# Performance work log

Hardware: AMD Instinct MI355X
Metric: run time of the kernel (lower is better)

The kernel has to match this reference:

```python
import jax, jax.numpy as jnp
import numpy as np

B, S, H = 2, 2048, 2048
NH, NKV, HD = 16, 4, 128
THETA = 10000.0


def _rope_cos_sin(seq_len, head_dim, theta, dtype):
    inv_freq = 1.0 / (theta ** (jnp.arange(0, head_dim, 2, dtype=jnp.float32) / head_dim))
    t = jnp.arange(seq_len, dtype=jnp.float32)
    freqs = t[:, None] * inv_freq[None, :]          # [S, HD/2]
    emb = jnp.concatenate([freqs, freqs], axis=-1)  # [S, HD]
    return jnp.cos(emb).astype(dtype), jnp.sin(emb).astype(dtype)


def _rotate_half(x):
    d = x.shape[-1] // 2
    return jnp.concatenate([-x[..., d:], x[..., :d]], axis=-1)


def setup_inputs() -> dict:
    key = jax.random.key(0)
    ks = jax.random.split(key, 5)
    x = jax.random.normal(ks[0], (B, S, H), dtype=jnp.float32)
    Wq = jax.random.normal(ks[1], (NH * HD, H), dtype=jnp.float32) * 0.02
    Wk = jax.random.normal(ks[2], (NKV * HD, H), dtype=jnp.float32) * 0.02
    Wv = jax.random.normal(ks[3], (NKV * HD, H), dtype=jnp.float32) * 0.02
    Wo = jax.random.normal(ks[4], (H, H), dtype=jnp.float32) * 0.02
    causal = jnp.tril(jnp.ones((S, S), dtype=bool))
    attention_mask = jnp.where(causal, 0.0, -1e9).astype(jnp.float32)[None, None]  # [1,1,S,S]
    return {"x": x, "attention_mask": attention_mask, "Wq": Wq, "Wk": Wk, "Wv": Wv, "Wo": Wo}


def reference(x, attention_mask, Wq, Wk, Wv, Wo):
    b, s, _ = x.shape
    q = (x @ Wq.T).reshape(b, s, NH, HD).transpose(0, 2, 1, 3)    # [b,nh,s,hd]
    k = (x @ Wk.T).reshape(b, s, NKV, HD).transpose(0, 2, 1, 3)   # [b,nkv,s,hd]
    v = (x @ Wv.T).reshape(b, s, NKV, HD).transpose(0, 2, 1, 3)
    cos, sin = _rope_cos_sin(s, HD, THETA, x.dtype)               # [s,hd] each
    cos = cos[None, None]; sin = sin[None, None]
    q = q * cos + _rotate_half(q) * sin
    k = k * cos + _rotate_half(k) * sin
    rep = NH // NKV
    k = jnp.repeat(k, rep, axis=1)                                 # [b,nh,s,hd]
    v = jnp.repeat(v, rep, axis=1)
    scores = jnp.einsum('bhqd,bhkd->bhqk', q, k) / jnp.sqrt(jnp.asarray(HD, x.dtype))
    scores = scores + attention_mask
    attn = jax.nn.softmax(scores, axis=-1)
    out = jnp.einsum('bhqk,bhkd->bhqd', attn, v)                   # [b,nh,s,hd]
    out = out.transpose(0, 2, 1, 3).reshape(b, s, NH * HD)
    return out @ Wo.T
```

## Files before the change

kernel.cpp:

```cpp
#include <hip/hip_runtime.h>

typedef unsigned short u16;
typedef __bf16 bf16x8 __attribute__((ext_vector_type(8)));
typedef float f32x4 __attribute__((ext_vector_type(4)));
typedef short s16x4 __attribute__((ext_vector_type(4)));

#define S_LEN  2048
#define NHEADS 16
#define NKVH   4
#define HDIM   128
#define BB     2
#define MROWS  4096
#define QKV_N  3072
#define HID    2048

__device__ __forceinline__ u16 f2b(float f) {
  union { float f; unsigned u; } x; x.f = f;
  unsigned r = x.u + 0x7fffu + ((x.u >> 16) & 1u);
  return (u16)(r >> 16);
}
__device__ __forceinline__ float b2f(u16 v) {
  union { unsigned u; float f; } x; x.u = ((unsigned)v) << 16;
  return x.f;
}
__device__ __forceinline__ void gload_lds16(const u16* g, u16* l) {
  __builtin_amdgcn_global_load_lds((__attribute__((address_space(1))) void*)g,
                                   (__attribute__((address_space(3))) void*)l,
                                   16, 0, 0);
}
__device__ __forceinline__ unsigned cvtpk(float lo, float hi) {
  unsigned r;
  asm("v_cvt_pk_bf16_f32 %0, %1, %2" : "=v"(r) : "v"(lo), "v"(hi));
  return r;
}
#if __has_builtin(__builtin_amdgcn_mfma_f32_16x16x16bf16_1k)
__device__ __forceinline__ f32x4 mfma16(s16x4 a, s16x4 b, f32x4 c) {
  return __builtin_amdgcn_mfma_f32_16x16x16bf16_1k(a, b, c, 0, 0, 0);
}
#else
__device__ __forceinline__ f32x4 mfma16(s16x4 a, s16x4 b, f32x4 c) {
  f32x4 d;
  asm volatile("v_mfma_f32_16x16x16_bf16 %0, %1, %2, %3"
               : "=v"(d) : "v"(a), "v"(b), "v"(c));
  return d;
}
#endif

#define SBAR() do { __builtin_amdgcn_sched_barrier(0); \
                    __builtin_amdgcn_s_barrier();      \
                    __builtin_amdgcn_sched_barrier(0); } while (0)

#define PB_X   8192
#define PB_WQ  (PB_X + 4096)
#define PB_WK  (PB_WQ + 1024)
#define PB_WV  (PB_WK + 1024)
#define PB_WO  (PB_WV + 4096)
#define PB_CS  (PB_WO + 512)
__global__ void k_prep(const float* __restrict__ x,
                       const float* __restrict__ Wq, const float* __restrict__ Wk,
                       const float* __restrict__ Wv, const float* __restrict__ Wo,
                       u16* __restrict__ xb, u16* __restrict__ Wqkvb,
                       u16* __restrict__ Wob, float* __restrict__ cs)
{
  const int bid = blockIdx.x, tid = threadIdx.x;
  const float* src; u16* dst; int i;
  if (bid < PB_X)       { i = bid * 256 + tid;            src = x;  dst = xb; }
  else if (bid < PB_WQ) { i = (bid - PB_X) * 256 + tid;   src = Wq; dst = Wqkvb; }
  else if (bid < PB_WK) { i = (bid - PB_WQ) * 256 + tid;  src = Wk; dst = Wqkvb + (size_t)2048 * HID; }
  else if (bid < PB_WV) { i = (bid - PB_WK) * 256 + tid;  src = Wv; dst = Wqkvb + (size_t)2560 * HID; }
  else if (bid < PB_WO) { i = (bid - PB_WV) * 256 + tid;  src = Wo; dst = Wob; }
  else {
    const int p = (bid - PB_WO) * 256 + tid;
    const int s = p >> 6, j = p & 63;
    float inv = expf(-(float)j * 0.14391156831212787f);
    float ang = (float)s * inv;
    float c, sn; sincosf(ang, &sn, &c);
    cs[p * 2 + 0] = c; cs[p * 2 + 1] = sn;
    return;
  }
  float4 v = ((const float4*)src)[i];
  ushort4 o;
  o.x = f2b(v.x); o.y = f2b(v.y); o.z = f2b(v.z); o.w = f2b(v.w);
  ((ushort4*)dst)[i] = o;
}

#define MFMA_GRP(AV, BV, MO, NO)                                              \
  __builtin_amdgcn_s_setprio(1);                                              \
  _Pragma("unroll") for (int kk = 0; kk < 2; ++kk)                            \
  _Pragma("unroll") for (int mm = 0; mm < 4; ++mm)                            \
  _Pragma("unroll") for (int nn = 0; nn < 2; ++nn)                            \
    acc[(MO) + mm][(NO) + nn] = __builtin_amdgcn_mfma_f32_16x16x32_bf16(      \
        AV[kk][mm], BV[kk][nn], acc[(MO) + mm][(NO) + nn], 0, 0, 0);          \
  __builtin_amdgcn_s_setprio(0);

template <int OUT_BF16>
__global__ __launch_bounds__(512, 2) void k_gemm256(
    const u16* __restrict__ A, const u16* __restrict__ Bm, void* __restrict__ Cv,
    int M, int N, int K)
{
  __shared__ u16 AL[2][2][8192];
  __shared__ u16 BL[2][2][8192];
  const int tid = threadIdx.x;
  const int wave = tid >> 6, lane = tid & 63;
  const int l15 = lane & 15, l4 = lane >> 4;
  const int wr = wave >> 2, wc = wave & 3;
  const int gx = gridDim.x;
  const int nwg = gx * gridDim.y;
  int bid = blockIdx.y * gx + blockIdx.x;
  bid = (bid & 7) * (nwg >> 3) + (bid >> 3);
  const int col0 = (bid % gx) * 256, row0 = (bid / gx) * 256;

  int srcOff[2], dstD[2];
#pragma unroll
  for (int li = 0; li < 2; ++li) {
    const int D = (li * 512 + tid) * 16;
    const int off_p = D & 1023, si = D >> 10;
    const int off_l = off_p ^ (((off_p >> 9) & 1) << 5);
    const int R = si >> 1, C = si & 1;
    const int row = R * 16 + (off_l >> 6);
    const int colb = C * 64 + (off_l & 63);
    srcOff[li] = row * K + (colb >> 1);
    dstD[li] = D;
  }
  const int laneoff = (l15 * 64 + l4 * 16) ^ ((l15 >> 3) << 5);

  auto stage = [&](const u16* __restrict__ G, int grow0, int kb, u16* lds) {
#pragma unroll
    for (int li = 0; li < 2; ++li)
      gload_lds16(G + (size_t)grow0 * K + kb + srcOff[li],
                  (u16*)((char*)lds + dstD[li]));
  };

  f32x4 acc[8][4];
#pragma unroll
  for (int m = 0; m < 8; ++m)
#pragma unroll
    for (int n = 0; n < 4; ++n) acc[m][n] = f32x4{0.f, 0.f, 0.f, 0.f};

  const int nk = K >> 6;
  stage(A,  row0,       0,  &AL[0][0][0]);
  stage(A,  row0 + 128, 0,  &AL[0][1][0]);
  stage(Bm, col0,       0,  &BL[0][0][0]);
  stage(Bm, col0 + 128, 0,  &BL[0][1][0]);
  stage(A,  row0,       64, &AL[1][0][0]);
  stage(A,  row0 + 128, 64, &AL[1][1][0]);
  asm volatile("s_waitcnt vmcnt(4)" ::: "memory");
  SBAR();

  for (int t = 0; t < nk; ++t) {
    const int bi = t & 1;
    const bool sB = (t + 1 < nk);
    const bool sA = (t + 2 < nk);
    const char* Ab = (const char*)&AL[bi][wr][0];
    const char* Bb = (const char*)&BL[bi][wc >> 1][0] + (wc & 1) * 8192;
    bf16x8 a0[2][4], a1[2][4], b0[2][2], b1[2][2];
#pragma unroll
    for (int kk = 0; kk < 2; ++kk)
#pragma unroll
      for (int m = 0; m < 4; ++m)
        a0[kk][m] = *(const bf16x8*)(Ab + m * 2048 + kk * 1024 + laneoff);
#pragma unroll
    for (int kk = 0; kk < 2; ++kk)
#pragma unroll
      for (int n = 0; n < 2; ++n)
        b0[kk][n] = *(const bf16x8*)(Bb + n * 2048 + kk * 1024 + laneoff);
    if (sB) stage(Bm, col0, (t + 1) * 64, &BL[bi ^ 1][0][0]);
    SBAR();
    MFMA_GRP(a0, b0, 0, 0);
    SBAR();
#pragma unroll
    for (int kk = 0; kk < 2; ++kk)
#pragma unroll
      for (int m = 0; m < 4; ++m)
        a1[kk][m] = *(const bf16x8*)(Ab + (m + 4) * 2048 + kk * 1024 + laneoff);
    if (sB) stage(Bm, col0 + 128, (t + 1) * 64, &BL[bi ^ 1][1][0]);
    SBAR();
    MFMA_GRP(a1, b0, 4, 0);
    SBAR();
#pragma unroll
    for (int kk = 0; kk < 2; ++kk)
#pragma unroll
      for (int n = 0; n < 2; ++n)
        b1[kk][n] = *(const bf16x8*)(Bb + (n + 2) * 2048 + kk * 1024 + laneoff);
    if (sA) stage(A, row0, (t + 2) * 64, &AL[bi][0][0]);
    SBAR();
    MFMA_GRP(a1, b1, 4, 2);
    SBAR();
    if (sA) {
      stage(A, row0 + 128, (t + 2) * 64, &AL[bi][1][0]);
      asm volatile("s_waitcnt vmcnt(4)" ::: "memory");
    } else if (sB) {
      asm volatile("s_waitcnt vmcnt(0)" ::: "memory");
    }
    SBAR();
    MFMA_GRP(a0, b1, 0, 2);
    SBAR();
  }

#pragma unroll
  for (int m = 0; m < 8; ++m) {
    const int r = row0 + wr * 128 + m * 16 + l4 * 4;
#pragma unroll
    for (int n = 0; n < 4; ++n) {
      const int c = col0 + wc * 64 + n * 16 + l15;
#pragma unroll
      for (int j = 0; j < 4; ++j) {
        const float v = acc[m][n][j];
        if (OUT_BF16) ((u16*)Cv)[(size_t)(r + j) * N + c] = f2b(v);
        else          ((float*)Cv)[(size_t)(r + j) * N + c] = v;
      }
    }
  }
}

template <int OUT_BF16>
__global__ __launch_bounds__(256) void k_gemm_bt(
    const u16* __restrict__ A, const u16* __restrict__ Bm, void* __restrict__ Cv,
    int M, int N, int K)
{
  __shared__ u16 Al[128 * 32];
  __shared__ u16 Bl[128 * 32];
  const int tid = threadIdx.x;
  const int wave = tid >> 6, lane = tid & 63;
  const int l15 = lane & 15, l4 = lane >> 4;
  const int wr = wave >> 1, wc = wave & 1;
  const int row0 = blockIdx.y * 128, col0 = blockIdx.x * 128;

  f32x4 zero = {0.f, 0.f, 0.f, 0.f};
  f32x4 acc[4][4];
#pragma unroll
  for (int m = 0; m < 4; ++m)
#pragma unroll
    for (int n = 0; n < 4; ++n) acc[m][n] = zero;

  const int e0 = lane * 8;
  for (int kb = 0; kb < K; kb += 32) {
#pragma unroll
    for (int it = 0; it < 2; ++it) {
      const int chunk = it * 4 + wave;
      const int e = chunk * 512 + e0;
      const int r = e >> 5, c = e & 31;
      gload_lds16(A + (size_t)(row0 + r) * K + kb + c, Al + chunk * 512);
      gload_lds16(Bm + (size_t)(col0 + r) * K + kb + c, Bl + chunk * 512);
    }
    __syncthreads();
    bf16x8 af[4], bfv[4];
#pragma unroll
    for (int m = 0; m < 4; ++m)
      af[m] = *(const bf16x8*)(Al + (wr * 64 + m * 16 + l15) * 32 + l4 * 8);
#pragma unroll
    for (int n = 0; n < 4; ++n)
      bfv[n] = *(const bf16x8*)(Bl + (wc * 64 + n * 16 + l15) * 32 + l4 * 8);
#pragma unroll
    for (int m = 0; m < 4; ++m)
#pragma unroll
      for (int n = 0; n < 4; ++n)
        acc[m][n] = __builtin_amdgcn_mfma_f32_16x16x32_bf16(af[m], bfv[n], acc[m][n], 0, 0, 0);
    __syncthreads();
  }
#pragma unroll
  for (int m = 0; m < 4; ++m) {
    const int r = row0 + wr * 64 + m * 16 + l4 * 4;
#pragma unroll
    for (int n = 0; n < 4; ++n) {
      const int c = col0 + wc * 64 + n * 16 + l15;
#pragma unroll
      for (int j = 0; j < 4; ++j) {
        const float v = acc[m][n][j];
        if (OUT_BF16) ((u16*)Cv)[(size_t)(r + j) * N + c] = f2b(v);
        else          ((float*)Cv)[(size_t)(r + j) * N + c] = v;
      }
    }
  }
}

__global__ __launch_bounds__(256) void k_ropev(
    const u16* __restrict__ qkv, const float* __restrict__ cs,
    u16* __restrict__ Qr, u16* __restrict__ Kr, u16* __restrict__ Vt)
{
  const int blk = blockIdx.x;
  const int b = blk >> 8, s0 = (blk & 255) << 3;
  const int tid = threadIdx.x;
  const float S2 = 0.08838834764831845f * 1.4426950408889634f;
#pragma unroll
  for (int p = tid; p < 8192; p += 256) {
    const int s = p >> 10, rem = p & 1023, h = rem >> 6, j = rem & 63;
    const int sg = s0 + s;
    const float c = cs[(sg * 64 + j) * 2], sn = cs[(sg * 64 + j) * 2 + 1];
    const u16* src = qkv + (size_t)(b * S_LEN + sg) * QKV_N + h * 128;
    const float x0 = b2f(src[j]), x1 = b2f(src[64 + j]);
    const size_t base = ((size_t)(b * NHEADS + h) * S_LEN + sg) * HDIM;
    Qr[base + j]      = f2b((x0 * c - x1 * sn) * S2);
    Qr[base + 64 + j] = f2b((x1 * c + x0 * sn) * S2);
  }
#pragma unroll
  for (int p = tid; p < 2048; p += 256) {
    const int s = p >> 8, rem = p & 255, h = rem >> 6, j = rem & 63;
    const int sg = s0 + s;
    const float c = cs[(sg * 64 + j) * 2], sn = cs[(sg * 64 + j) * 2 + 1];
    const u16* src = qkv + (size_t)(b * S_LEN + sg) * QKV_N + 2048 + h * 128;
    const float x0 = b2f(src[j]), x1 = b2f(src[64 + j]);
    const size_t base = ((size_t)(b * NKVH + h) * S_LEN + sg) * HDIM;
    Kr[base + j]      = f2b(x0 * c - x1 * sn);
    Kr[base + 64 + j] = f2b(x1 * c + x0 * sn);
  }
#pragma unroll
  for (int vi = 0; vi < 2; ++vi) {
    const int idx = vi * 256 + tid, h = idx >> 7, d = idx & 127;
    union { u16 u[8]; uint4 v; } bb;
#pragma unroll
    for (int s = 0; s < 8; ++s)
      bb.u[s] = qkv[(size_t)(b * S_LEN + s0 + s) * QKV_N + 2560 + idx];
    *(uint4*)(Vt + ((size_t)(b * NKVH + h) * HDIM + d) * S_LEN + s0) = bb.v;
  }
}

__device__ __forceinline__ void attn_qtile(
    int qt, int lastPhase,
    const u16* __restrict__ Q, const u16* __restrict__ Kg, const u16* __restrict__ Vg,
    u16* __restrict__ Out, int bh,
    u16* Kl0, u16* Kl1, u16* Vl0, u16* Vl1,
    const int (&ko)[4], const int (&vo)[4],
    int wave, int lane, int& cur)
{
  const int l15 = lane & 15, l4 = lane >> 4;
  const int b = bh >> 4, h = bh & 15;
  const int qw0 = qt * 64 + wave * 16;
  const u16* Qg = Q + ((size_t)bh * S_LEN + qw0) * HDIM;

  bf16x8 qf[4];
#pragma unroll
  for (int kc = 0; kc < 4; ++kc)
    qf[kc] = *(const bf16x8*)(Qg + l15 * HDIM + kc * 32 + l4 * 8);

  f32x4 zero = {0.f, 0.f, 0.f, 0.f};
  f32x4 oacc[8];
#pragma unroll
  for (int i = 0; i < 8; ++i) oacc[i] = zero;
  float m_r = -1e30f, l_p = 0.f;

  const int nt = qt + 1;
  const int qg = qw0 + l15;

  for (int t = 0; t < nt; ++t) {
    const int kt = t * 64;
    u16* Vb = cur ? Vl1 : Vl0;
#pragma unroll
    for (int it = 0; it < 4; ++it)
      gload_lds16(Vg + (size_t)vo[it] + kt, Vb + (it * 4 + wave) * 512);
    const int hasNext = (t + 1 < nt) || (!lastPhase);
    const int ktn = (t + 1 < nt) ? kt + 64 : 0;
    u16* Kn = cur ? Kl0 : Kl1;
    if (hasNext) {
#pragma unroll
      for (int it = 0; it < 4; ++it)
        gload_lds16(Kg + (size_t)ktn * HDIM + ko[it], Kn + (it * 4 + wave) * 512);
      asm volatile("s_waitcnt vmcnt(8)" ::: "memory");
    } else {
      asm volatile("s_waitcnt vmcnt(4)" ::: "memory");
    }
    SBAR();

    const char* Kb = (const char*)(cur ? Kl1 : Kl0);
    f32x4 s[4];
#pragma unroll
    for (int n = 0; n < 4; ++n) s[n] = zero;
    __builtin_amdgcn_s_setprio(1);
#pragma unroll
    for (int n = 0; n < 4; ++n) {
      const int row = n * 16 + l15;
#pragma unroll
      for (int kc = 0; kc < 4; ++kc) {
        const int ab = (row * 256 + kc * 64 + l4 * 16) ^ ((row & 7) << 4);
        bf16x8 kf = *(const bf16x8*)(Kb + ab);
        s[n] = __builtin_amdgcn_mfma_f32_16x16x32_bf16(kf, qf[kc], s[n], 0, 0, 0);
      }
    }
    __builtin_amdgcn_s_setprio(0);
    float sv[4][4];
    if (kt + 63 > qw0) {
#pragma unroll
      for (int n = 0; n < 4; ++n)
#pragma unroll
        for (int j = 0; j < 4; ++j) {
          float x = s[n][j];
          if (kt + n * 16 + l4 * 4 + j > qg) x = -1e30f;
          sv[n][j] = x;
        }
    } else {
#pragma unroll
      for (int n = 0; n < 4; ++n)
#pragma unroll
        for (int j = 0; j < 4; ++j) sv[n][j] = s[n][j];
    }
    float pm = sv[0][0];
#pragma unroll
    for (int n = 0; n < 4; ++n)
#pragma unroll
      for (int j = 0; j < 4; ++j) pm = fmaxf(pm, sv[n][j]);
    if (!__all(pm <= m_r + 11.5416f)) {
      float pf = fmaxf(pm, __shfl_xor(pm, 16, 64));
      pf = fmaxf(pf, __shfl_xor(pf, 32, 64));
      const float mn = fmaxf(m_r, pf);
      const float sc = exp2f(m_r - mn);
      m_r = mn;
      l_p *= sc;
      float scq[4];
#pragma unroll
      for (int j = 0; j < 4; ++j) scq[j] = __shfl(sc, l4 * 4 + j, 64);
#pragma unroll
      for (int nd = 0; nd < 8; ++nd)
#pragma unroll
        for (int j = 0; j < 4; ++j) oacc[nd][j] *= scq[j];
    }
    union { unsigned u[2]; s16x4 v; } a[4];
#pragma unroll
    for (int n = 0; n < 4; ++n) {
      const float p0 = exp2f(sv[n][0] - m_r);
      const float p1 = exp2f(sv[n][1] - m_r);
      const float p2 = exp2f(sv[n][2] - m_r);
      const float p3 = exp2f(sv[n][3] - m_r);
      l_p += (p0 + p1) + (p2 + p3);
      a[n].u[0] = cvtpk(p0, p1);
      a[n].u[1] = cvtpk(p2, p3);
    }
    if (hasNext) asm volatile("s_waitcnt vmcnt(4)" ::: "memory");
    else         asm volatile("s_waitcnt vmcnt(0)" ::: "memory");
    SBAR();
    __builtin_amdgcn_s_setprio(1);
#pragma unroll
    for (int nd = 0; nd < 8; ++nd) {
      const int d = nd * 16 + l15;
      const int rowb = d * 128, swz = (d & 7) << 4;
#pragma unroll
      for (int n = 0; n < 4; ++n) {
        const int ab = (rowb + n * 32 + l4 * 8) ^ swz;
        s16x4 vf = *(const s16x4*)((const char*)Vb + ab);
        oacc[nd] = mfma16(a[n].v, vf, oacc[nd]);
      }
    }
    __builtin_amdgcn_s_setprio(0);
    cur ^= 1;
  }

  l_p += __shfl_xor(l_p, 16, 64);
  l_p += __shfl_xor(l_p, 32, 64);
  float il[4];
#pragma unroll
  for (int j = 0; j < 4; ++j) il[j] = 1.f / __shfl(l_p, l4 * 4 + j, 64);
  const size_t obase = ((size_t)b * S_LEN + qw0 + l4 * 4) * HID + h * HDIM;
#pragma unroll
  for (int nd = 0; nd < 8; ++nd)
#pragma unroll
    for (int j = 0; j < 4; ++j)
      Out[obase + (size_t)j * HID + nd * 16 + l15] = f2b(oacc[nd][j] * il[j]);
}

__global__ __launch_bounds__(256) void k_attn(
    const u16* __restrict__ Q, const u16* __restrict__ Kr,
    const u16* __restrict__ Vt, u16* __restrict__ Out)
{
  __shared__ u16 Kl[2][64 * 128];
  __shared__ u16 Vl[2][128 * 64];
  const int tid = threadIdx.x;
  const int wave = tid >> 6, lane = tid & 63;
  const int bh = blockIdx.x;
  const int pairi = blockIdx.y;
  const int b = bh >> 4, h = bh & 15;
  const int kvh = h >> 2;

  const u16* Kg = Kr + (size_t)(b * NKVH + kvh) * S_LEN * HDIM;
  const u16* Vg = Vt + (size_t)(b * NKVH + kvh) * HDIM * S_LEN;

  int ko[4], vo[4];
#pragma unroll
  for (int it = 0; it < 4; ++it) {
    const int c = it * 4 + wave;
    const int L = c * 1024 + lane * 16;
    const int r = L >> 8;  const int w2 = (L & 255) ^ ((r & 7) << 4);
    ko[it] = r * HDIM + (w2 >> 1);
    const int d = L >> 7;  const int wv = (L & 127) ^ ((d & 7) << 4);
    vo[it] = d * S_LEN + (wv >> 1);
  }
#pragma unroll
  for (int it = 0; it < 4; ++it)
    gload_lds16(Kg + ko[it], &Kl[0][(it * 4 + wave) * 512]);

  int cur = 0;
  attn_qtile(31 - pairi, 0, Q, Kg, Vg, Out, bh, &Kl[0][0], &Kl[1][0],
             &Vl[0][0], &Vl[1][0], ko, vo, wave, lane, cur);
  attn_qtile(pairi,      1, Q, Kg, Vg, Out, bh, &Kl[0][0], &Kl[1][0],
             &Vl[0][0], &Vl[1][0], ko, vo, wave, lane, cur);
}

extern "C" void kernel_launch(void* const* d_in, const int* in_sizes, int n_in,
                              void* d_out, int out_size, void* d_ws, size_t ws_size,
                              hipStream_t stream)
{
  const float* x  = (const float*)d_in[0];
  const float* Wq = (const float*)d_in[2];
  const float* Wk = (const float*)d_in[3];
  const float* Wv = (const float*)d_in[4];
  const float* Wo = (const float*)d_in[5];
  float* out = (float*)d_out;

  u16* xb    = (u16*)d_ws;
  u16* Wqkvb = xb    + (size_t)MROWS * HID;
  u16* Wob   = Wqkvb + (size_t)QKV_N * HID;
  u16* qkv   = Wob   + (size_t)HID * HID;
  u16* Qr    = qkv   + (size_t)MROWS * QKV_N;
  u16* Kr    = Qr    + (size_t)BB * NHEADS * S_LEN * HDIM;
  u16* Vt    = Kr    + (size_t)BB * NKVH * S_LEN * HDIM;
  u16* attn  = Vt    + (size_t)BB * NKVH * S_LEN * HDIM;
  float* cs  = (float*)(attn + (size_t)MROWS * HID);

  k_prep<<<dim3(PB_CS), 256, 0, stream>>>(x, Wq, Wk, Wv, Wo, xb, Wqkvb, Wob, cs);
  k_gemm256<1><<<dim3(QKV_N / 256, MROWS / 256), 512, 0, stream>>>(xb, Wqkvb, qkv, MROWS, QKV_N, HID);
  k_ropev<<<dim3(BB * 256), 256, 0, stream>>>(qkv, cs, Qr, Kr, Vt);
  k_attn<<<dim3(BB * NHEADS, 16), 256, 0, stream>>>(Qr, Kr, Vt, attn);
  k_gemm_bt<0><<<dim3(HID / 128, MROWS / 128), 256, 0, stream>>>(attn, Wob, out, MROWS, HID, HID);
}
```

Baseline: 222.7 us.

## Restructure attention to 128-row query tiles with GQA-grouped block ordering

Each wave now handles 32 query rows (two 16-row MFMA fragments), so every K/V tile loaded into LDS feeds twice as many MFMAs. The paired long/short q-tile scheme is replaced by one 128-row tile per block, launched longest-first on a 1D grid where heads sharing a KV head sit in adjacent block ids, which should improve L2 reuse of K and V. K and V prefetch are now issued together after the QK MFMAs, and exp2f is swapped for raw v_exp_f32. The cost is higher register pressure from doubled accumulators and possible load imbalance, since the causal pairing that evened out work per block is gone.

```diff
diff --git a/kernel.cpp b/kernel.cpp
--- a/kernel.cpp
+++ b/kernel.cpp
@@ -31,6 +31,11 @@
 __device__ __forceinline__ unsigned cvtpk(float lo, float hi) {
   unsigned r;
   asm("v_cvt_pk_bf16_f32 %0, %1, %2" : "=v"(r) : "v"(lo), "v"(hi));
+  return r;
+}
+__device__ __forceinline__ float fexp2(float x) {
+  float r;
+  asm("v_exp_f32 %0, %1" : "=v"(r) : "v"(x));
   return r;
 }
 #if __has_builtin(__builtin_amdgcn_mfma_f32_16x16x16bf16_1k)
@@ -315,147 +320,6 @@
   }
 }
 
-__device__ __forceinline__ void attn_qtile(
-    int qt, int lastPhase,
-    const u16* __restrict__ Q, const u16* __restrict__ Kg, const u16* __restrict__ Vg,
-    u16* __restrict__ Out, int bh,
-    u16* Kl0, u16* Kl1, u16* Vl0, u16* Vl1,
-    const int (&ko)[4], const int (&vo)[4],
-    int wave, int lane, int& cur)
-{
-  const int l15 = lane & 15, l4 = lane >> 4;
-  const int b = bh >> 4, h = bh & 15;
-  const int qw0 = qt * 64 + wave * 16;
-  const u16* Qg = Q + ((size_t)bh * S_LEN + qw0) * HDIM;
-
-  bf16x8 qf[4];
-#pragma unroll
-  for (int kc = 0; kc < 4; ++kc)
-    qf[kc] = *(const bf16x8*)(Qg + l15 * HDIM + kc * 32 + l4 * 8);
-
-  f32x4 zero = {0.f, 0.f, 0.f, 0.f};
-  f32x4 oacc[8];
-#pragma unroll
-  for (int i = 0; i < 8; ++i) oacc[i] = zero;
-  float m_r = -1e30f, l_p = 0.f;
-
-  const int nt = qt + 1;
-  const int qg = qw0 + l15;
-
-  for (int t = 0; t < nt; ++t) {
-    const int kt = t * 64;
-    u16* Vb = cur ? Vl1 : Vl0;
-#pragma unroll
-    for (int it = 0; it < 4; ++it)
-      gload_lds16(Vg + (size_t)vo[it] + kt, Vb + (it * 4 + wave) * 512);
-    const int hasNext = (t + 1 < nt) || (!lastPhase);
-    const int ktn = (t + 1 < nt) ? kt + 64 : 0;
-    u16* Kn = cur ? Kl0 : Kl1;
-    if (hasNext) {
-#pragma unroll
-      for (int it = 0; it < 4; ++it)
-        gload_lds16(Kg + (size_t)ktn * HDIM + ko[it], Kn + (it * 4 + wave) * 512);
-      asm volatile("s_waitcnt vmcnt(8)" ::: "memory");
-    } else {
-      asm volatile("s_waitcnt vmcnt(4)" ::: "memory");
-    }
-    SBAR();
-
-    const char* Kb = (const char*)(cur ? Kl1 : Kl0);
-    f32x4 s[4];
-#pragma unroll
-    for (int n = 0; n < 4; ++n) s[n] = zero;
-    __builtin_amdgcn_s_setprio(1);
-#pragma unroll
-    for (int n = 0; n < 4; ++n) {
-      const int row = n * 16 + l15;
-#pragma unroll
-      for (int kc = 0; kc < 4; ++kc) {
-        const int ab = (row * 256 + kc * 64 + l4 * 16) ^ ((row & 7) << 4);
-        bf16x8 kf = *(const bf16x8*)(Kb + ab);
-        s[n] = __builtin_amdgcn_mfma_f32_16x16x32_bf16(kf, qf[kc], s[n], 0, 0, 0);
-      }
-    }
-    __builtin_amdgcn_s_setprio(0);
-    float sv[4][4];
-    if (kt + 63 > qw0) {
-#pragma unroll
-      for (int n = 0; n < 4; ++n)
-#pragma unroll
-        for (int j = 0; j < 4; ++j) {
-          float x = s[n][j];
-          if (kt + n * 16 + l4 * 4 + j > qg) x = -1e30f;
-          sv[n][j] = x;
-        }
-    } else {
-#pragma unroll
-      for (int n = 0; n < 4; ++n)
-#pragma unroll
-        for (int j = 0; j < 4; ++j) sv[n][j] = s[n][j];
-    }
-    float pm = sv[0][0];
-#pragma unroll
-    for (int n = 0; n < 4; ++n)
-#pragma unroll
-      for (int j = 0; j < 4; ++j) pm = fmaxf(pm, sv[n][j]);
-    if (!__all(pm <= m_r + 11.5416f)) {
-      float pf = fmaxf(pm, __shfl_xor(pm, 16, 64));
-      pf = fmaxf(pf, __shfl_xor(pf, 32, 64));
-      const float mn = fmaxf(m_r, pf);
-      const float sc = exp2f(m_r - mn);
-      m_r = mn;
-      l_p *= sc;
-      float scq[4];
-#pragma unroll
-      for (int j = 0; j < 4; ++j) scq[j] = __shfl(sc, l4 * 4 + j, 64);
-#pragma unroll
-      for (int nd = 0; nd < 8; ++nd)
-#pragma unroll
-        for (int j = 0; j < 4; ++j) oacc[nd][j] *= scq[j];
-    }
-    union { unsigned u[2]; s16x4 v; } a[4];
-#pragma unroll
-    for (int n = 0; n < 4; ++n) {
-      const float p0 = exp2f(sv[n][0] - m_r);
-      const float p1 = exp2f(sv[n][1] - m_r);
-      const float p2 = exp2f(sv[n][2] - m_r);
-      const float p3 = exp2f(sv[n][3] - m_r);
-      l_p += (p0 + p1) + (p2 + p3);
-      a[n].u[0] = cvtpk(p0, p1);
-      a[n].u[1] = cvtpk(p2, p3);
-    }
-    if (hasNext) asm volatile("s_waitcnt vmcnt(4)" ::: "memory");
-    else         asm volatile("s_waitcnt vmcnt(0)" ::: "memory");
-    SBAR();
-    __builtin_amdgcn_s_setprio(1);
-#pragma unroll
-    for (int nd = 0; nd < 8; ++nd) {
-      const int d = nd * 16 + l15;
-      const int rowb = d * 128, swz = (d & 7) << 4;
-#pragma unroll
-      for (int n = 0; n < 4; ++n) {
-        const int ab = (rowb + n * 32 + l4 * 8) ^ swz;
-        s16x4 vf = *(const s16x4*)((const char*)Vb + ab);
-        oacc[nd] = mfma16(a[n].v, vf, oacc[nd]);
-      }
-    }
-    __builtin_amdgcn_s_setprio(0);
-    cur ^= 1;
-  }
-
-  l_p += __shfl_xor(l_p, 16, 64);
-  l_p += __shfl_xor(l_p, 32, 64);
-  float il[4];
-#pragma unroll
-  for (int j = 0; j < 4; ++j) il[j] = 1.f / __shfl(l_p, l4 * 4 + j, 64);
-  const size_t obase = ((size_t)b * S_LEN + qw0 + l4 * 4) * HID + h * HDIM;
-#pragma unroll
-  for (int nd = 0; nd < 8; ++nd)
-#pragma unroll
-    for (int j = 0; j < 4; ++j)
-      Out[obase + (size_t)j * HID + nd * 16 + l15] = f2b(oacc[nd][j] * il[j]);
-}
-
 __global__ __launch_bounds__(256) void k_attn(
     const u16* __restrict__ Q, const u16* __restrict__ Kr,
     const u16* __restrict__ Vt, u16* __restrict__ Out)
@@ -464,10 +328,12 @@
   __shared__ u16 Vl[2][128 * 64];
   const int tid = threadIdx.x;
   const int wave = tid >> 6, lane = tid & 63;
-  const int bh = blockIdx.x;
-  const int pairi = blockIdx.y;
-  const int b = bh >> 4, h = bh & 15;
-  const int kvh = h >> 2;
+  const int l15 = lane & 15, l4 = lane >> 4;
+  const int bid = blockIdx.x;
+  const int xg = bid & 7;
+  const int b = xg >> 2, kvh = xg & 3;
+  const int h = kvh * 4 + ((bid >> 3) & 3);
+  const int qt = 15 - (bid >> 5);
 
   const u16* Kg = Kr + (size_t)(b * NKVH + kvh) * S_LEN * HDIM;
   const u16* Vg = Vt + (size_t)(b * NKVH + kvh) * HDIM * S_LEN;
@@ -482,15 +348,169 @@
     const int d = L >> 7;  const int wv = (L & 127) ^ ((d & 7) << 4);
     vo[it] = d * S_LEN + (wv >> 1);
   }
+
+  const int qw0 = qt * 128 + wave * 32;
+  const u16* Qg = Q + ((size_t)(b * NHEADS + h) * S_LEN + qw0) * HDIM;
+
+  bf16x8 qf[2][4];
+#pragma unroll
+  for (int mq = 0; mq < 2; ++mq)
+#pragma unroll
+    for (int kc = 0; kc < 4; ++kc)
+      qf[mq][kc] = *(const bf16x8*)(Qg + (mq * 16 + l15) * HDIM + kc * 32 + l4 * 8);
+
+  f32x4 zero = {0.f, 0.f, 0.f, 0.f};
+  f32x4 oacc[2][8];
+#pragma unroll
+  for (int mq = 0; mq < 2; ++mq)
+#pragma unroll
+    for (int i = 0; i < 8; ++i) oacc[mq][i] = zero;
+  float m_r[2] = {-1e30f, -1e30f}, l_p[2] = {0.f, 0.f};
+
+  const int nt = 2 * qt + 2;
+  const int qgl = qw0 + l15;
+  int cur = 0;
+
 #pragma unroll
   for (int it = 0; it < 4; ++it)
     gload_lds16(Kg + ko[it], &Kl[0][(it * 4 + wave) * 512]);
-
-  int cur = 0;
-  attn_qtile(31 - pairi, 0, Q, Kg, Vg, Out, bh, &Kl[0][0], &Kl[1][0],
-             &Vl[0][0], &Vl[1][0], ko, vo, wave, lane, cur);
-  attn_qtile(pairi,      1, Q, Kg, Vg, Out, bh, &Kl[0][0], &Kl[1][0],
-             &Vl[0][0], &Vl[1][0], ko, vo, wave, lane, cur);
+#pragma unroll
+  for (int it = 0; it < 4; ++it)
+    gload_lds16(Vg + (size_t)vo[it], &Vl[0][(it * 4 + wave) * 512]);
+
+  for (int t = 0; t < nt; ++t) {
+    const int kt = t * 64;
+    asm volatile("s_waitcnt vmcnt(4)" ::: "memory");
+    SBAR();
+    const char* Kb = (const char*)(cur ? &Kl[1][0] : &Kl[0][0]);
+    const char* Vb = (const char*)(cur ? &Vl[1][0] : &Vl[0][0]);
+    f32x4 s[2][4];
+#pragma unroll
+    for (int mq = 0; mq < 2; ++mq)
+#pragma unroll
+      for (int n = 0; n < 4; ++n) s[mq][n] = zero;
+    __builtin_amdgcn_s_setprio(1);
+#pragma unroll
+    for (int n = 0; n < 4; ++n) {
+      const int row = n * 16 + l15;
+#pragma unroll
+      for (int kc = 0; kc < 4; ++kc) {
+        const int ab = (row * 256 + kc * 64 + l4 * 16) ^ ((row & 7) << 4);
+        bf16x8 kf = *(const bf16x8*)(Kb + ab);
+        s[0][n] = __builtin_amdgcn_mfma_f32_16x16x32_bf16(kf, qf[0][kc], s[0][n], 0, 0, 0);
+        s[1][n] = __builtin_amdgcn_mfma_f32_16x16x32_bf16(kf, qf[1][kc], s[1][n], 0, 0, 0);
+      }
+    }
+    __builtin_amdgcn_s_setprio(0);
+    const int hasNext = (t + 1 < nt);
+    if (hasNext) {
+      const int ktn = kt + 64;
+      u16* Kn = cur ? &Kl[0][0] : &Kl[1][0];
+      u16* Vn = cur ? &Vl[0][0] : &Vl[1][0];
+#pragma unroll
+      for (int it = 0; it < 4; ++it)
+        gload_lds16(Kg + (size_t)ktn * HDIM + ko[it], Kn + (it * 4 + wave) * 512);
+#pragma unroll
+      for (int it = 0; it < 4; ++it)
+        gload_lds16(Vg + (size_t)vo[it] + ktn, Vn + (it * 4 + wave) * 512);
+    }
+    float sv[2][4][4];
+    if (kt + 63 > qw0) {
+#pragma unroll
+      for (int mq = 0; mq < 2; ++mq)
+#pragma unroll
+        for (int n = 0; n < 4; ++n)
+#pragma unroll
+          for (int j = 0; j < 4; ++j) {
+            float x = s[mq][n][j];
+            if (kt + n * 16 + l4 * 4 + j > qgl + mq * 16) x = -1e30f;
+            sv[mq][n][j] = x;
+          }
+    } else {
+#pragma unroll
+      for (int mq = 0; mq < 2; ++mq)
+#pragma unroll
+        for (int n = 0; n < 4; ++n)
+#pragma unroll
+          for (int j = 0; j < 4; ++j) sv[mq][n][j] = s[mq][n][j];
+    }
+    float pm[2];
+#pragma unroll
+    for (int mq = 0; mq < 2; ++mq) {
+      pm[mq] = sv[mq][0][0];
+#pragma unroll
+      for (int n = 0; n < 4; ++n)
+#pragma unroll
+        for (int j = 0; j < 4; ++j) pm[mq] = fmaxf(pm[mq], sv[mq][n][j]);
+    }
+    const bool ok = (pm[0] <= m_r[0] + 11.5416f) && (pm[1] <= m_r[1] + 11.5416f);
+    if (!__all(ok)) {
+#pragma unroll
+      for (int mq = 0; mq < 2; ++mq) {
+        float pf = fmaxf(pm[mq], __shfl_xor(pm[mq], 16, 64));
+        pf = fmaxf(pf, __shfl_xor(pf, 32, 64));
+        const float mn = fmaxf(m_r[mq], pf);
+        const float sc = fexp2(m_r[mq] - mn);
+        m_r[mq] = mn;
+        l_p[mq] *= sc;
+        float scq[4];
+#pragma unroll
+        for (int j = 0; j < 4; ++j) scq[j] = __shfl(sc, l4 * 4 + j, 64);
+#pragma unroll
+        for (int nd = 0; nd < 8; ++nd)
+#pragma unroll
+          for (int j = 0; j < 4; ++j) oacc[mq][nd][j] *= scq[j];
+      }
+    }
+    union { unsigned u[2]; s16x4 v; } a[2][4];
+#pragma unroll
+    for (int mq = 0; mq < 2; ++mq)
+#pragma unroll
+      for (int n = 0; n < 4; ++n) {
+        const float p0 = fexp2(sv[mq][n][0] - m_r[mq]);
+        const float p1 = fexp2(sv[mq][n][1] - m_r[mq]);
+        const float p2 = fexp2(sv[mq][n][2] - m_r[mq]);
+        const float p3 = fexp2(sv[mq][n][3] - m_r[mq]);
+        l_p[mq] += (p0 + p1) + (p2 + p3);
+        a[mq][n].u[0] = cvtpk(p0, p1);
+        a[mq][n].u[1] = cvtpk(p2, p3);
+      }
+    if (hasNext) asm volatile("s_waitcnt vmcnt(8)" ::: "memory");
+    else         asm volatile("s_waitcnt vmcnt(0)" ::: "memory");
+    SBAR();
+    __builtin_amdgcn_s_setprio(1);
+#pragma unroll
+    for (int nd = 0; nd < 8; ++nd) {
+      const int d = nd * 16 + l15;
+      const int rowb = d * 128, swz = (d & 7) << 4;
+#pragma unroll
+      for (int n = 0; n < 4; ++n) {
+        const int ab = (rowb + n * 32 + l4 * 8) ^ swz;
+        s16x4 vf = *(const s16x4*)(Vb + ab);
+        oacc[0][nd] = mfma16(a[0][n].v, vf, oacc[0][nd]);
+        oacc[1][nd] = mfma16(a[1][n].v, vf, oacc[1][nd]);
+      }
+    }
+    __builtin_amdgcn_s_setprio(0);
+    cur ^= 1;
+  }
+
+#pragma unroll
+  for (int mq = 0; mq < 2; ++mq) {
+    float lp = l_p[mq];
+    lp += __shfl_xor(lp, 16, 64);
+    lp += __shfl_xor(lp, 32, 64);
+    float il[4];
+#pragma unroll
+    for (int j = 0; j < 4; ++j) il[j] = 1.f / __shfl(lp, l4 * 4 + j, 64);
+    const size_t obase =
+        ((size_t)b * S_LEN + qw0 + mq * 16 + l4 * 4) * HID + h * HDIM;
+#pragma unroll
+    for (int nd = 0; nd < 8; ++nd)
+#pragma unroll
+      for (int j = 0; j < 4; ++j)
+        Out[obase + (size_t)j * HID + nd * 16 + l15] = f2b(oacc[mq][nd][j] * il[j]);
+  }
 }
 
 extern "C" void kernel_launch(void* const* d_in, const int* in_sizes, int n_in,
@@ -517,6 +537,6 @@
   k_prep<<<dim3(PB_CS), 256, 0, stream>>>(x, Wq, Wk, Wv, Wo, xb, Wqkvb, Wob, cs);
   k_gemm256<1><<<dim3(QKV_N / 256, MROWS / 256), 512, 0, stream>>>(xb, Wqkvb, qkv, MROWS, QKV_N, HID);
   k_ropev<<<dim3(BB * 256), 256, 0, stream>>>(qkv, cs, Qr, Kr, Vt);
-  k_attn<<<dim3(BB * NHEADS, 16), 256, 0, stream>>>(Qr, Kr, Vt, attn);
+  k_attn<<<dim3(512), 256, 0, stream>>>(Qr, Kr, Vt, attn);
   k_gemm_bt<0><<<dim3(HID / 128, MROWS / 128), 256, 0, stream>>>(attn, Wob, out, MROWS, HID, HID);
 }
```

New measurement: 234.3 us. 1.05x slower.
